# Performance work log

Measured on AMD Instinct MI355X. Metric: run time of the kernel, lower is better.

Reference implementation:

```python
import jax, jax.numpy as jnp
import numpy as np

B, Q, K, H, DV = 16, 256, 256, 256, 256


def setup_inputs() -> dict:
    key = jax.random.key(0)
    ks = jax.random.split(key, 6)
    return {
        "queries": jax.random.normal(ks[0], (B, Q, H), dtype=jnp.float32),
        "keys": jax.random.normal(ks[1], (B, K, H), dtype=jnp.float32),
        "values": jax.random.normal(ks[2], (B, K, DV), dtype=jnp.float32),
        "W_q": jax.random.normal(ks[3], (H, H), dtype=jnp.float32) / np.sqrt(H),
        "W_k": jax.random.normal(ks[4], (H, H), dtype=jnp.float32) / np.sqrt(H),
        "w_v": jax.random.normal(ks[5], (H,), dtype=jnp.float32) / np.sqrt(H),
    }


def reference(queries, keys, values, W_q, W_k, w_v):
    # Linear projections (nn.Linear: x @ W.T), bias-free
    q = jnp.einsum("bqd,hd->bqh", queries, W_q)  # [B,Q,H]
    k = jnp.einsum("bkd,hd->bkh", keys, W_k)      # [B,K,H]
    # Broadcast add -> tanh -> scalar projection
    features = jnp.tanh(q[:, :, None, :] + k[:, None, :, :])  # [B,Q,K,H]
    scores = jnp.einsum("bqkh,h->bqk", features, w_v)          # [B,Q,K]
    attn = jax.nn.softmax(scores, axis=-1)                      # [B,Q,K]
    return jnp.einsum("bqk,bkv->bqv", attn, values)            # [B,Q,DV]
```

## Files before the change

kernel.cpp:

```cpp
#include <hip/hip_runtime.h>

#define Bn 16
#define Qn 256
#define Kn 256
#define Hn 256
#define DVn 256

constexpr float C2    = 2.8853900817779268f;
constexpr float LOG2E = 1.4426950408889634f;

typedef __attribute__((ext_vector_type(8))) short bf16x8;
typedef __attribute__((ext_vector_type(4))) float f32x4;

__device__ __forceinline__ float fast_exp2(float x) { return __builtin_amdgcn_exp2f(x); }
__device__ __forceinline__ float fast_rcp(float x)  { return __builtin_amdgcn_rcpf(x); }

__device__ __forceinline__ unsigned short f2bf(float x) {
    unsigned u = __float_as_uint(x);
    u += 0x7fffu + ((u >> 16) & 1u);
    return (unsigned short)(u >> 16);
}

__device__ __forceinline__ bf16x8 cvt8(const float* p) {
    float4 x0 = *(const float4*)p;
    float4 x1 = *(const float4*)(p + 4);
    bf16x8 r;
    r[0] = (short)f2bf(x0.x); r[1] = (short)f2bf(x0.y);
    r[2] = (short)f2bf(x0.z); r[3] = (short)f2bf(x0.w);
    r[4] = (short)f2bf(x1.x); r[5] = (short)f2bf(x1.y);
    r[6] = (short)f2bf(x1.z); r[7] = (short)f2bf(x1.w);
    return r;
}

__global__ __launch_bounds__(256)
void proj_mfma_kernel(const float* __restrict__ q, const float* __restrict__ kx,
                      const float* __restrict__ wq, const float* __restrict__ wk,
                      const float* __restrict__ V,
                      float* __restrict__ Eq, unsigned short* __restrict__ Ekb,
                      float* __restrict__ Vp)
{
    const int tid  = threadIdx.x;
    const int wvid = tid >> 6, lane = tid & 63;
    const int bid  = blockIdx.x;
    const int m0   = (bid >> 1) * 16;
    const int n0   = (bid & 1) * 128 + wvid * 32;
    const bool isQ = (m0 < 4096);
    const int r16  = lane & 15, q8 = (lane >> 4) * 8;

    const float* Xrow = (isQ ? q + (size_t)(m0 + r16) * 256
                             : kx + (size_t)(m0 - 4096 + r16) * 256) + q8;
    bf16x8 afr[8];
    #pragma unroll
    for (int s = 0; s < 8; ++s) afr[s] = cvt8(Xrow + s * 32);

    const float* Wbase = isQ ? wq : wk;
    f32x4 acc[2];
    #pragma unroll
    for (int nt = 0; nt < 2; ++nt) {
        const float* Wrow = Wbase + (size_t)(n0 + nt * 16 + r16) * 256 + q8;
        f32x4 c = {0.f, 0.f, 0.f, 0.f};
        #pragma unroll
        for (int s = 0; s < 8; ++s) {
            bf16x8 bfr = cvt8(Wrow + s * 32);
            c = __builtin_amdgcn_mfma_f32_16x16x32_bf16(afr[s], bfr, c, 0, 0, 0);
        }
        acc[nt] = c;
    }
    const int rbase = (lane >> 4) * 4;
    #pragma unroll
    for (int nt = 0; nt < 2; ++nt) {
        const int n = n0 + nt * 16 + r16;
        #pragma unroll
        for (int r = 0; r < 4; ++r) {
            const int m = m0 + rbase + r;
            const float val = fast_exp2(C2 * acc[nt][r]);
            if (isQ) {
                Eq[(size_t)m * 256 + n] = val;
            } else {
                const int kr = m - 4096, b = kr >> 8, kk = kr & 255;
                Ekb[(((size_t)(b * 64 + (n >> 2))) * 256 + kk) * 4 + (n & 3)] = f2bf(val);
            }
        }
    }
    {
        const int p   = bid * 256 + tid;
        const int bk4 = p >> 8, dv = p & 255;
        const int b   = bk4 >> 6, k4 = bk4 & 63;
        const float* src = V + ((size_t)(b * Kn + 4 * k4)) * DVn + dv;
        float4 o;
        o.x = src[0 * DVn]; o.y = src[1 * DVn]; o.z = src[2 * DVn]; o.w = src[3 * DVn];
        *(float4*)(Vp + (size_t)p * 4) = o;
    }
}

__global__ __launch_bounds__(512, 8)
void fused_attn_kernel(const float* __restrict__ Eq, const unsigned short* __restrict__ Ekb,
                       const float* __restrict__ wv, const float* __restrict__ Vp,
                       float* __restrict__ out)
{
    const int b    = blockIdx.y;
    const int q0   = blockIdx.x * 4;
    const int tid  = threadIdx.x;
    const int kk   = tid & 255;
    const int half = tid >> 8;
    const int halfu = __builtin_amdgcn_readfirstlane(half);

    __shared__ __align__(16) float sEq[4 * 256];
    __shared__ __align__(16) float sWv[256];
    __shared__ __align__(16) float sPart[2][256][4];
    __shared__ __align__(16) float sPv[256 * 4];
    __shared__ float sredM[4][8];
    __shared__ float sredS[4][8];

    {
        const float* eqb = Eq + (size_t)(b * Qn + q0) * Hn;
        if (tid < 256) {
            const int qq = tid >> 6, h4 = (tid & 63) * 4;
            *(float4*)&sEq[qq * 256 + h4] = *(const float4*)(eqb + qq * 256 + h4);
        } else if (tid < 320) {
            const int j = (tid - 256) * 4;
            *(float4*)&sWv[j] = *(const float4*)(wv + j);
        }
    }
    __syncthreads();

    float sc[4] = {0.f, 0.f, 0.f, 0.f};
    const uint2* ekp = (const uint2*)Ekb + (size_t)b * 16384 + (size_t)(halfu * 32) * 256 + kk;
    uint2 e[4];
    #pragma unroll
    for (int g = 0; g < 4; ++g) e[g] = ekp[g * 256];
    for (int it = 0; it < 8; ++it) {
        uint2 en[4];
        if (it < 7) {
            #pragma unroll
            for (int g = 0; g < 4; ++g) en[g] = ekp[(4 * (it + 1) + g) * 256];
        }
        const int h0 = halfu * 128 + it * 16;
        float ek[16];
        #pragma unroll
        for (int g = 0; g < 4; ++g) {
            ek[4*g+0] = __uint_as_float(e[g].x << 16);
            ek[4*g+1] = __uint_as_float(e[g].x & 0xFFFF0000u);
            ek[4*g+2] = __uint_as_float(e[g].y << 16);
            ek[4*g+3] = __uint_as_float(e[g].y & 0xFFFF0000u);
        }
        #pragma unroll
        for (int g = 0; g < 4; ++g) {
            const float4 wa = *(const float4*)&sWv[h0 + 4 * g];
            #pragma unroll
            for (int qq = 0; qq < 4; ++qq) {
                const float4 ea = *(const float4*)&sEq[qq * 256 + h0 + 4 * g];
                float a = sc[qq];
                a = fmaf(wa.x, fast_rcp(fmaf(ea.x, ek[4*g+0], 1.f)), a);
                a = fmaf(wa.y, fast_rcp(fmaf(ea.y, ek[4*g+1], 1.f)), a);
                a = fmaf(wa.z, fast_rcp(fmaf(ea.z, ek[4*g+2], 1.f)), a);
                a = fmaf(wa.w, fast_rcp(fmaf(ea.w, ek[4*g+3], 1.f)), a);
                sc[qq] = a;
            }
        }
        #pragma unroll
        for (int g = 0; g < 4; ++g) e[g] = en[g];
    }

    *(float4*)&sPart[half][kk][0] = make_float4(sc[0], sc[1], sc[2], sc[3]);
    __syncthreads();
    const float4 pa = *(const float4*)&sPart[0][kk][0];
    const float4 pb = *(const float4*)&sPart[1][kk][0];
    float tot[4] = {pa.x + pb.x, pa.y + pb.y, pa.z + pb.z, pa.w + pb.w};

    const int w = tid >> 6, lane = tid & 63;
    #pragma unroll
    for (int qq = 0; qq < 4; ++qq) {
        tot[qq] = -2.0f * tot[qq];
        float mx = tot[qq];
        #pragma unroll
        for (int off = 32; off; off >>= 1) mx = fmaxf(mx, __shfl_xor(mx, off, 64));
        if (lane == 0) sredM[qq][w] = mx;
    }
    __syncthreads();
    float pq[4];
    #pragma unroll
    for (int qq = 0; qq < 4; ++qq) {
        float mx = sredM[qq][0];
        #pragma unroll
        for (int i = 1; i < 8; ++i) mx = fmaxf(mx, sredM[qq][i]);
        pq[qq] = fast_exp2(LOG2E * (tot[qq] - mx));
        float s = pq[qq];
        #pragma unroll
        for (int off = 32; off; off >>= 1) s += __shfl_xor(s, off, 64);
        if (lane == 0) sredS[qq][w] = s;
    }
    if (halfu == 0) *(float4*)&sPv[kk * 4] = make_float4(pq[0], pq[1], pq[2], pq[3]);
    __syncthreads();
    float rinv[4];
    #pragma unroll
    for (int qq = 0; qq < 4; ++qq) {
        float s = sredS[qq][0];
        #pragma unroll
        for (int i = 1; i < 8; ++i) s += sredS[qq][i];
        rinv[qq] = fast_rcp(0.5f * s);
    }

    float acc[4] = {0.f, 0.f, 0.f, 0.f};
    const float4* vp = (const float4*)Vp + (size_t)b * 64 * 256 + (size_t)(halfu * 32) * 256 + kk;
    float4 vv = vp[0];
    for (int k4 = 0; k4 < 32; ++k4) {
        float4 vn;
        if (k4 < 31) vn = vp[(k4 + 1) * 256];
        const int kb = (halfu * 32 + k4) * 4;
        const float vj[4] = {vv.x, vv.y, vv.z, vv.w};
        #pragma unroll
        for (int j = 0; j < 4; ++j) {
            const float4 p4 = *(const float4*)&sPv[(kb + j) * 4];
            acc[0] = fmaf(p4.x, vj[j], acc[0]);
            acc[1] = fmaf(p4.y, vj[j], acc[1]);
            acc[2] = fmaf(p4.z, vj[j], acc[2]);
            acc[3] = fmaf(p4.w, vj[j], acc[3]);
        }
        vv = vn;
    }
    *(float4*)&sPart[half][kk][0] = make_float4(acc[0], acc[1], acc[2], acc[3]);
    __syncthreads();
    {
        const int dv = kk;
        const float4 u0 = *(const float4*)&sPart[0][dv][0];
        const float4 u1 = *(const float4*)&sPart[1][dv][0];
        float a0, a1;
        if (halfu == 0) { a0 = u0.x + u1.x; a1 = u0.y + u1.y; }
        else            { a0 = u0.z + u1.z; a1 = u0.w + u1.w; }
        float* ob = out + (size_t)(b * Qn + q0 + 2 * halfu) * DVn + dv;
        ob[0]   = a0 * rinv[2 * halfu + 0];
        ob[DVn] = a1 * rinv[2 * halfu + 1];
    }
}

extern "C" void kernel_launch(void* const* d_in, const int* in_sizes, int n_in,
                              void* d_out, int out_size, void* d_ws, size_t ws_size,
                              hipStream_t stream) {
    const float* queries = (const float*)d_in[0];
    const float* keys    = (const float*)d_in[1];
    const float* values  = (const float*)d_in[2];
    const float* W_q     = (const float*)d_in[3];
    const float* W_k     = (const float*)d_in[4];
    const float* w_v     = (const float*)d_in[5];
    float* out = (float*)d_out;

    float*          Eq  = (float*)d_ws;
    unsigned short* Ekb = (unsigned short*)(Eq + (size_t)Bn * Qn * Hn);
    float*          Vp  = (float*)(Ekb + (size_t)Bn * Kn * Hn);

    proj_mfma_kernel<<<dim3(1024), 256, 0, stream>>>(queries, keys, W_q, W_k, values,
                                                     Eq, Ekb, Vp);
    fused_attn_kernel<<<dim3(64, 16), 512, 0, stream>>>(Eq, Ekb, w_v, Vp, out);
}
```

Before: 158.4 us.

## Drop the split-H halves; one thread per key covers the full hidden dimension

The block drops from 512 to 256 threads, and each thread now walks the full 256-wide hidden dimension for its key. This removes the cross-half partial-sum exchange through shared memory, along with two barriers and the split reduction in the PV step. The trade-off is half as many threads per block, twice the serial loop length per thread, and launch bounds lowered to 256 threads with 4 waves.

```diff
diff --git a/kernel.cpp b/kernel.cpp
--- a/kernel.cpp
+++ b/kernel.cpp
@@ -93,68 +93,56 @@
     }
 }
 
-__global__ __launch_bounds__(512, 8)
+__global__ __launch_bounds__(256, 4)
 void fused_attn_kernel(const float* __restrict__ Eq, const unsigned short* __restrict__ Ekb,
                        const float* __restrict__ wv, const float* __restrict__ Vp,
                        float* __restrict__ out)
 {
-    const int b    = blockIdx.y;
-    const int q0   = blockIdx.x * 4;
-    const int tid  = threadIdx.x;
-    const int kk   = tid & 255;
-    const int half = tid >> 8;
-    const int halfu = __builtin_amdgcn_readfirstlane(half);
+    const int b   = blockIdx.y;
+    const int q0  = blockIdx.x * 4;
+    const int tid = threadIdx.x;
 
     __shared__ __align__(16) float sEq[4 * 256];
     __shared__ __align__(16) float sWv[256];
-    __shared__ __align__(16) float sPart[2][256][4];
     __shared__ __align__(16) float sPv[256 * 4];
-    __shared__ float sredM[4][8];
-    __shared__ float sredS[4][8];
+    __shared__ float sredM[4][4];
+    __shared__ float sredS[4][4];
 
     {
         const float* eqb = Eq + (size_t)(b * Qn + q0) * Hn;
-        if (tid < 256) {
-            const int qq = tid >> 6, h4 = (tid & 63) * 4;
-            *(float4*)&sEq[qq * 256 + h4] = *(const float4*)(eqb + qq * 256 + h4);
-        } else if (tid < 320) {
-            const int j = (tid - 256) * 4;
-            *(float4*)&sWv[j] = *(const float4*)(wv + j);
-        }
+        const int qq = tid >> 6, h4 = (tid & 63) * 4;
+        *(float4*)&sEq[qq * 256 + h4] = *(const float4*)(eqb + qq * 256 + h4);
+        if (tid < 64) *(float4*)&sWv[tid * 4] = *(const float4*)(wv + tid * 4);
     }
     __syncthreads();
 
     float sc[4] = {0.f, 0.f, 0.f, 0.f};
-    const uint2* ekp = (const uint2*)Ekb + (size_t)b * 16384 + (size_t)(halfu * 32) * 256 + kk;
+    const uint2* ekp = (const uint2*)Ekb + (size_t)b * 16384 + tid;
     uint2 e[4];
     #pragma unroll
     for (int g = 0; g < 4; ++g) e[g] = ekp[g * 256];
-    for (int it = 0; it < 8; ++it) {
+    for (int it = 0; it < 16; ++it) {
         uint2 en[4];
-        if (it < 7) {
+        if (it < 15) {
             #pragma unroll
             for (int g = 0; g < 4; ++g) en[g] = ekp[(4 * (it + 1) + g) * 256];
         }
-        const int h0 = halfu * 128 + it * 16;
-        float ek[16];
+        const int h0 = it * 16;
         #pragma unroll
         for (int g = 0; g < 4; ++g) {
-            ek[4*g+0] = __uint_as_float(e[g].x << 16);
-            ek[4*g+1] = __uint_as_float(e[g].x & 0xFFFF0000u);
-            ek[4*g+2] = __uint_as_float(e[g].y << 16);
-            ek[4*g+3] = __uint_as_float(e[g].y & 0xFFFF0000u);
-        }
-        #pragma unroll
-        for (int g = 0; g < 4; ++g) {
+            float ek0 = __uint_as_float(e[g].x << 16);
+            float ek1 = __uint_as_float(e[g].x & 0xFFFF0000u);
+            float ek2 = __uint_as_float(e[g].y << 16);
+            float ek3 = __uint_as_float(e[g].y & 0xFFFF0000u);
             const float4 wa = *(const float4*)&sWv[h0 + 4 * g];
             #pragma unroll
             for (int qq = 0; qq < 4; ++qq) {
                 const float4 ea = *(const float4*)&sEq[qq * 256 + h0 + 4 * g];
                 float a = sc[qq];
-                a = fmaf(wa.x, fast_rcp(fmaf(ea.x, ek[4*g+0], 1.f)), a);
-                a = fmaf(wa.y, fast_rcp(fmaf(ea.y, ek[4*g+1], 1.f)), a);
-                a = fmaf(wa.z, fast_rcp(fmaf(ea.z, ek[4*g+2], 1.f)), a);
-                a = fmaf(wa.w, fast_rcp(fmaf(ea.w, ek[4*g+3], 1.f)), a);
+                a = fmaf(wa.x, fast_rcp(fmaf(ea.x, ek0, 1.f)), a);
+                a = fmaf(wa.y, fast_rcp(fmaf(ea.y, ek1, 1.f)), a);
+                a = fmaf(wa.z, fast_rcp(fmaf(ea.z, ek2, 1.f)), a);
+                a = fmaf(wa.w, fast_rcp(fmaf(ea.w, ek3, 1.f)), a);
                 sc[qq] = a;
             }
         }
@@ -162,17 +150,11 @@
         for (int g = 0; g < 4; ++g) e[g] = en[g];
     }
 
-    *(float4*)&sPart[half][kk][0] = make_float4(sc[0], sc[1], sc[2], sc[3]);
-    __syncthreads();
-    const float4 pa = *(const float4*)&sPart[0][kk][0];
-    const float4 pb = *(const float4*)&sPart[1][kk][0];
-    float tot[4] = {pa.x + pb.x, pa.y + pb.y, pa.z + pb.z, pa.w + pb.w};
-
     const int w = tid >> 6, lane = tid & 63;
     #pragma unroll
     for (int qq = 0; qq < 4; ++qq) {
-        tot[qq] = -2.0f * tot[qq];
-        float mx = tot[qq];
+        sc[qq] = -2.0f * sc[qq];
+        float mx = sc[qq];
         #pragma unroll
         for (int off = 32; off; off >>= 1) mx = fmaxf(mx, __shfl_xor(mx, off, 64));
         if (lane == 0) sredM[qq][w] = mx;
@@ -181,37 +163,31 @@
     float pq[4];
     #pragma unroll
     for (int qq = 0; qq < 4; ++qq) {
-        float mx = sredM[qq][0];
-        #pragma unroll
-        for (int i = 1; i < 8; ++i) mx = fmaxf(mx, sredM[qq][i]);
-        pq[qq] = fast_exp2(LOG2E * (tot[qq] - mx));
+        const float mx = fmaxf(fmaxf(sredM[qq][0], sredM[qq][1]),
+                               fmaxf(sredM[qq][2], sredM[qq][3]));
+        pq[qq] = fast_exp2(LOG2E * (sc[qq] - mx));
         float s = pq[qq];
         #pragma unroll
         for (int off = 32; off; off >>= 1) s += __shfl_xor(s, off, 64);
         if (lane == 0) sredS[qq][w] = s;
     }
-    if (halfu == 0) *(float4*)&sPv[kk * 4] = make_float4(pq[0], pq[1], pq[2], pq[3]);
+    *(float4*)&sPv[tid * 4] = make_float4(pq[0], pq[1], pq[2], pq[3]);
     __syncthreads();
     float rinv[4];
     #pragma unroll
-    for (int qq = 0; qq < 4; ++qq) {
-        float s = sredS[qq][0];
-        #pragma unroll
-        for (int i = 1; i < 8; ++i) s += sredS[qq][i];
-        rinv[qq] = fast_rcp(0.5f * s);
-    }
+    for (int qq = 0; qq < 4; ++qq)
+        rinv[qq] = fast_rcp(sredS[qq][0] + sredS[qq][1] + sredS[qq][2] + sredS[qq][3]);
 
     float acc[4] = {0.f, 0.f, 0.f, 0.f};
-    const float4* vp = (const float4*)Vp + (size_t)b * 64 * 256 + (size_t)(halfu * 32) * 256 + kk;
+    const float4* vp = (const float4*)Vp + (size_t)b * 64 * 256 + tid;
     float4 vv = vp[0];
-    for (int k4 = 0; k4 < 32; ++k4) {
+    for (int k4 = 0; k4 < 64; ++k4) {
         float4 vn;
-        if (k4 < 31) vn = vp[(k4 + 1) * 256];
-        const int kb = (halfu * 32 + k4) * 4;
+        if (k4 < 63) vn = vp[(k4 + 1) * 256];
         const float vj[4] = {vv.x, vv.y, vv.z, vv.w};
         #pragma unroll
         for (int j = 0; j < 4; ++j) {
-            const float4 p4 = *(const float4*)&sPv[(kb + j) * 4];
+            const float4 p4 = *(const float4*)&sPv[(4 * k4 + j) * 4];
             acc[0] = fmaf(p4.x, vj[j], acc[0]);
             acc[1] = fmaf(p4.y, vj[j], acc[1]);
             acc[2] = fmaf(p4.z, vj[j], acc[2]);
@@ -219,19 +195,11 @@
         }
         vv = vn;
     }
-    *(float4*)&sPart[half][kk][0] = make_float4(acc[0], acc[1], acc[2], acc[3]);
-    __syncthreads();
-    {
-        const int dv = kk;
-        const float4 u0 = *(const float4*)&sPart[0][dv][0];
-        const float4 u1 = *(const float4*)&sPart[1][dv][0];
-        float a0, a1;
-        if (halfu == 0) { a0 = u0.x + u1.x; a1 = u0.y + u1.y; }
-        else            { a0 = u0.z + u1.z; a1 = u0.w + u1.w; }
-        float* ob = out + (size_t)(b * Qn + q0 + 2 * halfu) * DVn + dv;
-        ob[0]   = a0 * rinv[2 * halfu + 0];
-        ob[DVn] = a1 * rinv[2 * halfu + 1];
-    }
+    float* ob = out + (size_t)(b * Qn + q0) * DVn + tid;
+    ob[0 * DVn] = acc[0] * rinv[0];
+    ob[1 * DVn] = acc[1] * rinv[1];
+    ob[2 * DVn] = acc[2] * rinv[2];
+    ob[3 * DVn] = acc[3] * rinv[3];
 }
 
 extern "C" void kernel_launch(void* const* d_in, const int* in_sizes, int n_in,
@@ -251,5 +219,5 @@
 
     proj_mfma_kernel<<<dim3(1024), 256, 0, stream>>>(queries, keys, W_q, W_k, values,
                                                      Eq, Ekb, Vp);
-    fused_attn_kernel<<<dim3(64, 16), 512, 0, stream>>>(Eq, Ekb, w_v, Vp, out);
-}
+    fused_attn_kernel<<<dim3(64, 16), 256, 0, stream>>>(Eq, Ekb, w_v, Vp, out);
+}
```

New measurement: 136.7 us. 13.7% less time.
